# Performance work log

Measured on AMD Instinct MI355X. Metric: run time of the kernel, lower is better.

## Reference

```python
import jax, jax.numpy as jnp
import numpy as np

NUM_QUBITS = 22
NUM_LAYERS = 4
DIM = 2 ** NUM_QUBITS


def _apply_1q(state, U, q):
    # state: flat [2^n]; apply 2x2 unitary U on wire q (wire 0 = most significant)
    s = state.reshape(2 ** q, 2, -1)
    return jnp.einsum('ab,ibj->iaj', U, s).reshape(-1)


def _apply_cnot_adj(state, q):
    # CNOT with control q, target q+1 (adjacent wires)
    s = state.reshape(2 ** q, 2, 2, -1)
    s = jnp.stack([s[:, 0], s[:, 1, ::-1]], axis=1)
    return s.reshape(-1)


def _rot_mats(theta_x, theta_y, theta_z):
    cx = jnp.cos(theta_x / 2).astype(jnp.complex64)
    sx = jnp.sin(theta_x / 2).astype(jnp.complex64)
    RX = jnp.stack([jnp.stack([cx, -1j * sx]), jnp.stack([-1j * sx, cx])])
    cy = jnp.cos(theta_y / 2).astype(jnp.complex64)
    sy = jnp.sin(theta_y / 2).astype(jnp.complex64)
    RY = jnp.stack([jnp.stack([cy, -sy]), jnp.stack([sy, cy])])
    tz = theta_z.astype(jnp.complex64)
    zero = jnp.zeros((), jnp.complex64)
    RZ = jnp.stack([jnp.stack([jnp.exp(-1j * tz / 2), zero]),
                    jnp.stack([zero, jnp.exp(1j * tz / 2)])])
    return RX, RY, RZ


def _circuit(params, state):
    for l in range(NUM_LAYERS):
        for q in range(NUM_QUBITS):
            RX, RY, RZ = _rot_mats(params[l, q, 0], params[l, q, 1], params[l, q, 2])
            state = _apply_1q(state, RX, q)
            state = _apply_1q(state, RY, q)
            state = _apply_1q(state, RZ, q)
        for q in range(NUM_QUBITS - 1):
            state = _apply_cnot_adj(state, q)
    # <Z_q> for each qubit
    probs = jnp.abs(state) ** 2
    expvals = []
    for q in range(NUM_QUBITS):
        p = probs.reshape(2 ** q, 2, -1)
        expvals.append(p[:, 0].sum() - p[:, 1].sum())
    return jnp.stack(expvals).astype(jnp.float32)


def setup_inputs() -> dict:
    key = jax.random.key(0)
    k1, k2, k3 = jax.random.split(key, 3)
    params = jax.random.normal(k1, (NUM_LAYERS, NUM_QUBITS, 3), dtype=jnp.float32)
    state_re = jax.random.normal(k2, (DIM,), dtype=jnp.float32)
    state_im = jax.random.normal(k3, (DIM,), dtype=jnp.float32)
    return {"params": params, "state_re": state_re, "state_im": state_im}


def reference(params, state_re, state_im):
    state = (state_re + 1j * state_im).astype(jnp.complex64)
    state = state / jnp.sqrt(jnp.sum(jnp.abs(state) ** 2))
    return _circuit(params, state)
```

## Files before the change

### kernel.cpp

```cpp
#include <hip/hip_runtime.h>
#include <math.h>

#define NQ 22
#define DIM (1u << NQ)

typedef float v2f __attribute__((ext_vector_type(2)));


__device__ __forceinline__ unsigned igray(unsigned x) {
  x ^= x >> 1; x ^= x >> 2; x ^= x >> 4; x ^= x >> 8; x ^= x >> 16;
  return x;
}

__global__ void k_gates(const float* __restrict__ params, float* __restrict__ U) {
  int t = blockIdx.x * blockDim.x + threadIdx.x;
  if (t >= 88) return;
  const float* p = params + t * 3;
  double hx = 0.5 * (double)p[0], hy = 0.5 * (double)p[1], hz = 0.5 * (double)p[2];
  double cx = cos(hx), sx = sin(hx);
  double cy = cos(hy), sy = sin(hy);
  double cz = cos(hz), sz = sin(hz);
  double m00r = cy * cx, m00i = sy * sx;
  double m01r = -sy * cx, m01i = -cy * sx;
  double m10r = sy * cx, m10i = -cy * sx;
  double m11r = cy * cx, m11i = -sy * sx;
  float* o = U + t * 8;
  o[0] = (float)(cz * m00r + sz * m00i); o[1] = (float)(cz * m00i - sz * m00r);
  o[2] = (float)(cz * m01r + sz * m01i); o[3] = (float)(cz * m01i - sz * m01r);
  o[4] = (float)(cz * m10r - sz * m10i); o[5] = (float)(cz * m10i + sz * m10r);
  o[6] = (float)(cz * m11r - sz * m11i); o[7] = (float)(cz * m11i + sz * m11r);
}

template <int NP>
__device__ __forceinline__ void apply_bit0(v2f RE[NP], v2f IM[NP], const float* __restrict__ u) {
  float u0 = u[0], u1 = u[1], u2 = u[2], u3 = u[3], u4 = u[4], u5 = u[5], u6 = u[6], u7 = u[7];
#pragma unroll
  for (int k = 0; k < NP; ++k) {
    float a0r = RE[k].x, a0i = IM[k].x, a1r = RE[k].y, a1i = IM[k].y;
    float n0r = u0 * a0r - u1 * a0i + u2 * a1r - u3 * a1i;
    float n0i = u0 * a0i + u1 * a0r + u2 * a1i + u3 * a1r;
    float n1r = u4 * a0r - u5 * a0i + u6 * a1r - u7 * a1i;
    float n1i = u4 * a0i + u5 * a0r + u6 * a1i + u7 * a1r;
    RE[k].x = n0r; IM[k].x = n0i; RE[k].y = n1r; IM[k].y = n1i;
  }
}

template <int NP, int PB>
__device__ __forceinline__ void apply_bitP(v2f RE[NP], v2f IM[NP], const float* __restrict__ u) {
  float u0 = u[0], u1 = u[1], u2 = u[2], u3 = u[3], u4 = u[4], u5 = u[5], u6 = u[6], u7 = u[7];
#pragma unroll
  for (int m = 0; m < NP / 2; ++m) {
    int k0 = ((m >> PB) << (PB + 1)) | (m & ((1 << PB) - 1));
    int k1 = k0 | (1 << PB);
    v2f a0r = RE[k0], a0i = IM[k0], a1r = RE[k1], a1i = IM[k1];
    v2f n0r = u0 * a0r - u1 * a0i + u2 * a1r - u3 * a1i;
    v2f n0i = u0 * a0i + u1 * a0r + u2 * a1i + u3 * a1r;
    v2f n1r = u4 * a0r - u5 * a0i + u6 * a1r - u7 * a1i;
    v2f n1i = u4 * a0i + u5 * a0r + u6 * a1i + u7 * a1r;
    RE[k0] = n0r; IM[k0] = n0i; RE[k1] = n1r; IM[k1] = n1i;
  }
}

__device__ __forceinline__ void apply4p(v2f RE[8], v2f IM[8], const float* __restrict__ U,
                                        int l, int wtop) {
  const float* base = U + ((l * 22 + wtop) << 3);
  apply_bit0<8>(RE, IM, base);
  apply_bitP<8, 0>(RE, IM, base - 8);
  apply_bitP<8, 1>(RE, IM, base - 16);
  apply_bitP<8, 2>(RE, IM, base - 24);
}

__device__ __forceinline__ void apply5p(v2f RE[16], v2f IM[16], const float* __restrict__ U,
                                        int l, int wtop) {
  const float* base = U + ((l * 22 + wtop) << 3);
  apply_bit0<16>(RE, IM, base);
  apply_bitP<16, 0>(RE, IM, base - 8);
  apply_bitP<16, 1>(RE, IM, base - 16);
  apply_bitP<16, 2>(RE, IM, base - 24);
  apply_bitP<16, 3>(RE, IM, base - 32);
}

template <typename WI, typename RI>
__device__ __forceinline__ void xchgP(float2* lds2, v2f RE[8], v2f IM[8], WI wi, RI ri) {
  __syncthreads();
#pragma unroll
  for (int d = 0; d < 16; ++d) {
    float2 a;
    if (d & 1) a = make_float2(RE[d >> 1].y, IM[d >> 1].y);
    else       a = make_float2(RE[d >> 1].x, IM[d >> 1].x);
    lds2[wi(d)] = a;
  }
  __syncthreads();
#pragma unroll
  for (int d = 0; d < 16; ++d) {
    float2 a = lds2[ri(d)];
    if (d & 1) { RE[d >> 1].y = a.x; IM[d >> 1].y = a.y; }
    else       { RE[d >> 1].x = a.x; IM[d >> 1].x = a.y; }
  }
}

__global__ __launch_bounds__(256, 4) void k_passA(const float* __restrict__ srcRe,
                                                  const float* __restrict__ srcIm,
                                                  const float2* __restrict__ src2,
                                                  float2* __restrict__ dst,
                                                  const float* __restrict__ U,
                                                  int layer, int first) {
  __shared__ float2 lds2[4096];
  const int t = threadIdx.x;
  const unsigned bid = blockIdx.x;
  const unsigned H = (bid & 7u) * (gridDim.x >> 3) + (bid >> 3);
  v2f RE[8], IM[8];
  if (first) {
    const unsigned jbase = (H << 12) | ((unsigned)t << 4);
    const float4* r4 = (const float4*)(srcRe + jbase);
    const float4* i4 = (const float4*)(srcIm + jbase);
#pragma unroll
    for (int k = 0; k < 4; ++k) {
      float4 r = r4[k], m = i4[k];
      RE[2 * k].x     = r.x; RE[2 * k].y     = r.y;
      IM[2 * k].x     = m.x; IM[2 * k].y     = m.y;
      RE[2 * k + 1].x = r.z; RE[2 * k + 1].y = r.w;
      IM[2 * k + 1].x = m.z; IM[2 * k + 1].y = m.w;
    }
  } else {
    const float4* s4 = (const float4*)(src2 + (((size_t)H << 12) | ((size_t)t << 4)));
#pragma unroll
    for (int k = 0; k < 8; ++k) {
      float4 a = s4[k];
      RE[k].x = a.x; IM[k].x = a.y;
      RE[k].y = a.z; IM[k].y = a.w;
    }
  }
  auto wA = [&](int d) { unsigned j = ((unsigned)t << 4) | (unsigned)d; return (int)(j ^ (j >> 4)); };
  auto rB = [&](int d) { unsigned j = (((unsigned)t >> 4) << 8) | ((unsigned)d << 4) | ((unsigned)t & 15); return (int)(j ^ (j >> 4)); };
  auto rC = [&](int d) { unsigned j = ((unsigned)d << 8) | (unsigned)t; return (int)(j ^ (j >> 4)); };

  apply4p(RE, IM, U, layer, 21);
  xchgP(lds2, RE, IM, wA, rB);
  apply4p(RE, IM, U, layer, 17);
  xchgP(lds2, RE, IM, rB, rC);
  apply4p(RE, IM, U, layer, 13);
  float2* dp = dst + (((size_t)H << 3) | (unsigned)(t & 7));
#pragma unroll
  for (int d = 0; d < 16; ++d) {
    float2 a;
    if (d & 1) a = make_float2(RE[d >> 1].y, IM[d >> 1].y);
    else       a = make_float2(RE[d >> 1].x, IM[d >> 1].x);
    dp[(((size_t)d << 5) | (unsigned)(t >> 3)) << 13] = a;
  }
}

__device__ __forceinline__ int pbf(unsigned e) {
  return (int)(e ^ (((e >> 8) & 7u) << 3));
}

__global__ __launch_bounds__(256, 2) void k_passB(const float2* __restrict__ src,
                                                  float2* __restrict__ dst,
                                                  const float* __restrict__ U,
                                                  int layer) {
  __shared__ float2 lds2[8192];
  const int t = threadIdx.x;
  const unsigned c = (unsigned)(t & 7), u = (unsigned)(t >> 3);
  const unsigned bid = blockIdx.x;
  const unsigned mid = (bid & 7u) * (gridDim.x >> 3) + (bid >> 3);
  const float2* sp = src + (((size_t)mid << 13) | c);
  v2f RE[16], IM[16];
#pragma unroll
  for (int d = 0; d < 32; ++d) {
    unsigned h = u | ((unsigned)d << 5);
    float2 a = sp[(size_t)h << 3];
    if (d & 1) { RE[d >> 1].y = a.x; IM[d >> 1].y = a.y; }
    else       { RE[d >> 1].x = a.x; IM[d >> 1].x = a.y; }
  }
  apply5p(RE, IM, U, layer, 4);
#pragma unroll
  for (int d = 0; d < 32; ++d) {
    unsigned e = ((u | ((unsigned)d << 5)) << 3) | c;
    float2 a;
    if (d & 1) a = make_float2(RE[d >> 1].y, IM[d >> 1].y);
    else       a = make_float2(RE[d >> 1].x, IM[d >> 1].x);
    lds2[pbf(e)] = a;
  }
  __syncthreads();
#pragma unroll
  for (int d = 0; d < 32; ++d) {
    unsigned e = (((unsigned)d | (u << 5)) << 3) | c;
    float2 a = lds2[pbf(e)];
    if (d & 1) { RE[d >> 1].y = a.x; IM[d >> 1].y = a.y; }
    else       { RE[d >> 1].x = a.x; IM[d >> 1].x = a.y; }
  }
  apply5p(RE, IM, U, layer, 9);
  const unsigned Tb = igray((u << 17) | (mid << 3) | c);
#pragma unroll
  for (int d = 0; d < 32; ++d) {
    float2 a;
    if (d & 1) a = make_float2(RE[d >> 1].y, IM[d >> 1].y);
    else       a = make_float2(RE[d >> 1].x, IM[d >> 1].x);
    dst[Tb ^ igray((unsigned)d << 12)] = a;
  }
}

__global__ __launch_bounds__(256, 2) void k_passB_ev(const float2* __restrict__ src,
                                                     const float* __restrict__ U,
                                                     float* __restrict__ partials,
                                                     int layer) {
  __shared__ float2 lds2[8192];
  const int t = threadIdx.x;
  const unsigned c = (unsigned)(t & 7), u = (unsigned)(t >> 3);
  const unsigned bid = blockIdx.x;
  const unsigned mid = (bid & 7u) * (gridDim.x >> 3) + (bid >> 3);
  const float2* sp = src + (((size_t)mid << 13) | c);
  v2f RE[16], IM[16];
#pragma unroll
  for (int d = 0; d < 32; ++d) {
    unsigned h = u | ((unsigned)d << 5);
    float2 a = sp[(size_t)h << 3];
    if (d & 1) { RE[d >> 1].y = a.x; IM[d >> 1].y = a.y; }
    else       { RE[d >> 1].x = a.x; IM[d >> 1].x = a.y; }
  }
  apply5p(RE, IM, U, layer, 4);
#pragma unroll
  for (int d = 0; d < 32; ++d) {
    unsigned e = ((u | ((unsigned)d << 5)) << 3) | c;
    float2 a;
    if (d & 1) a = make_float2(RE[d >> 1].y, IM[d >> 1].y);
    else       a = make_float2(RE[d >> 1].x, IM[d >> 1].x);
    lds2[pbf(e)] = a;
  }
  __syncthreads();
#pragma unroll
  for (int d = 0; d < 32; ++d) {
    unsigned e = (((unsigned)d | (u << 5)) << 3) | c;
    float2 a = lds2[pbf(e)];
    if (d & 1) { RE[d >> 1].y = a.x; IM[d >> 1].y = a.y; }
    else       { RE[d >> 1].x = a.x; IM[d >> 1].x = a.y; }
  }
  apply5p(RE, IM, U, layer, 9);

  v2f PS[16];
#pragma unroll
  for (int k = 0; k < 16; ++k) PS[k] = RE[k] * RE[k] + IM[k] * IM[k];
  v2f S4[8], B4[8];
#pragma unroll
  for (int k = 0; k < 8; ++k) { S4[k] = PS[k] + PS[k + 8]; B4[k] = PS[k] - PS[k + 8]; }
  float Tot = 0.f, W4 = 0.f;
#pragma unroll
  for (int k = 0; k < 8; ++k) { Tot += S4[k].x + S4[k].y; W4 += B4[k].x + B4[k].y; }
  v2f B3[4];
#pragma unroll
  for (int k = 0; k < 4; ++k) B3[k] = B4[k] - B4[k + 4];
  float W3 = (B3[0].x + B3[0].y) + (B3[1].x + B3[1].y) + (B3[2].x + B3[2].y) + (B3[3].x + B3[3].y);
  v2f B2[2];
  B2[0] = B3[0] - B3[2]; B2[1] = B3[1] - B3[3];
  float W2 = (B2[0].x + B2[0].y) + (B2[1].x + B2[1].y);
  v2f B1 = B2[0] - B2[1];
  float W1 = B1.x + B1.y;
  float W0 = B1.x - B1.y;

  unsigned lowfull = (mid << 3) | c;
  unsigned y = lowfull; y ^= y >> 1; y ^= y >> 2; y ^= y >> 4; y ^= y >> 8;
  unsigned pu = (unsigned)__popc(u) & 1u;
  float acc[22];
#pragma unroll
  for (int q = 0; q <= 4; ++q)
    acc[q] = ((unsigned)__popc(u >> (4 - q)) & 1u) ? -Tot : Tot;
  {
    float W[5] = {W0, W1, W2, W3, W4};
#pragma unroll
    for (int q = 5; q <= 9; ++q)
      acc[q] = pu ? -W[9 - q] : W[9 - q];
  }
#pragma unroll
  for (int q = 10; q <= 21; ++q)
    acc[q] = (((y >> (21 - q)) ^ pu) & 1u) ? -W0 : W0;

  __syncthreads();
  float* red = (float*)lds2;
  const int lane = t & 63, wv = t >> 6;
#pragma unroll
  for (int q = 0; q < 22; ++q) {
    float s = acc[q];
    for (int off = 32; off > 0; off >>= 1) s += __shfl_down(s, off, 64);
    if (lane == 0) red[wv * 23 + q] = s;
  }
  {
    float s = Tot;
    for (int off = 32; off > 0; off >>= 1) s += __shfl_down(s, off, 64);
    if (lane == 0) red[wv * 23 + 22] = s;
  }
  __syncthreads();
  if (t < 23) {
    float s = 0.f;
#pragma unroll
    for (int w = 0; w < 4; ++w) s += red[w * 23 + t];
    partials[t * 512 + mid] = s;
  }
}

__global__ void k_final(const float* __restrict__ partials, float* __restrict__ out) {
  __shared__ double res[32];
  const int t = threadIdx.x;
  const int r = t >> 3, l8 = t & 7;
  if (r < 23) {
    double s = 0.0;
    const float* p = partials + r * 512 + l8 * 64;
    for (int k = 0; k < 64; ++k) s += (double)p[k];
    for (int off = 4; off > 0; off >>= 1) s += __shfl_down(s, off, 8);
    if (l8 == 0) res[r] = s;
  }
  __syncthreads();
  if (t < 22) out[t] = (float)(res[t] / res[22]);
}

extern "C" void kernel_launch(void* const* d_in, const int* in_sizes, int n_in,
                              void* d_out, int out_size, void* d_ws, size_t ws_size,
                              hipStream_t stream) {
  const float* params = (const float*)d_in[0];
  const float* sre = (const float*)d_in[1];
  const float* sim = (const float*)d_in[2];
  float* out = (float*)d_out;
  char* ws = (char*)d_ws;
  float* U = (float*)ws;
  float* partials = (float*)(ws + 4096);
  float2* buf0 = (float2*)(ws + 131072);
  float2* buf1 = buf0 + DIM;

  k_gates<<<1, 128, 0, stream>>>(params, U);
  k_passA<<<1024, 256, 0, stream>>>(sre, sim, nullptr, buf0, U, 0, 1);
  k_passB<<<512, 256, 0, stream>>>(buf0, buf1, U, 0);
  for (int l = 1; l < 3; ++l) {
    k_passA<<<1024, 256, 0, stream>>>(nullptr, nullptr, buf1, buf0, U, l, 0);
    k_passB<<<512, 256, 0, stream>>>(buf0, buf1, U, l);
  }
  k_passA<<<1024, 256, 0, stream>>>(nullptr, nullptr, buf1, buf0, U, 3, 0);
  k_passB_ev<<<512, 256, 0, stream>>>(buf0, U, partials, 3);
  k_final<<<1, 256, 0, stream>>>(partials, out);
}
```

Before: 202.3 us.

## Restructure passB to use float4 accesses and three-stage LDS exchange

```diff
diff --git a/kernel.cpp b/kernel.cpp
--- a/kernel.cpp
+++ b/kernel.cpp
@@ -70,16 +70,6 @@
   apply_bitP<8, 2>(RE, IM, base - 24);
 }
 
-__device__ __forceinline__ void apply5p(v2f RE[16], v2f IM[16], const float* __restrict__ U,
-                                        int l, int wtop) {
-  const float* base = U + ((l * 22 + wtop) << 3);
-  apply_bit0<16>(RE, IM, base);
-  apply_bitP<16, 0>(RE, IM, base - 8);
-  apply_bitP<16, 1>(RE, IM, base - 16);
-  apply_bitP<16, 2>(RE, IM, base - 24);
-  apply_bitP<16, 3>(RE, IM, base - 32);
-}
-
 template <typename WI, typename RI>
 __device__ __forceinline__ void xchgP(float2* lds2, v2f RE[8], v2f IM[8], WI wi, RI ri) {
   __syncthreads();
@@ -150,53 +140,84 @@
   }
 }
 
-__device__ __forceinline__ int pbf(unsigned e) {
-  return (int)(e ^ (((e >> 8) & 7u) << 3));
+
+template <bool EV>
+__device__ __forceinline__ void passB_core(const float2* __restrict__ src,
+                                           const float* __restrict__ U,
+                                           float4* lds4, v2f RE[16], v2f IM[16],
+                                           unsigned c2, unsigned u6, unsigned mid,
+                                           int layer) {
+  const float4* sp4 = (const float4*)src + (((size_t)mid << 12) | c2);
+#pragma unroll
+  for (int k = 0; k < 16; ++k) {
+    float4 a = sp4[((unsigned)k << 8) | (u6 << 2)];
+    RE[k].x = a.x; RE[k].y = a.z;
+    IM[k].x = a.y; IM[k].y = a.w;
+  }
+  const float* B = U + layer * 22 * 8;
+  apply_bitP<16, 0>(RE, IM, B + 3 * 8);
+  apply_bitP<16, 1>(RE, IM, B + 2 * 8);
+  apply_bitP<16, 2>(RE, IM, B + 1 * 8);
+  apply_bitP<16, 3>(RE, IM, B + 0 * 8);
+#pragma unroll
+  for (int k = 0; k < 16; ++k) {
+    unsigned s = ((unsigned)k << 8) | (u6 << 2) | c2;
+    s ^= (s >> 6) & 7u;
+    lds4[s] = make_float4(RE[k].x, IM[k].x, RE[k].y, IM[k].y);
+  }
+  __syncthreads();
+#pragma unroll
+  for (int k = 0; k < 16; ++k) {
+    unsigned s = ((unsigned)k << 2) | (u6 << 6) | c2;
+    s ^= (s >> 6) & 7u;
+    float4 a = lds4[s];
+    RE[k].x = a.x; IM[k].x = a.y;
+    RE[k].y = a.z; IM[k].y = a.w;
+  }
+  apply_bitP<16, 0>(RE, IM, B + 9 * 8);
+  apply_bitP<16, 1>(RE, IM, B + 8 * 8);
+  apply_bitP<16, 2>(RE, IM, B + 7 * 8);
+  apply_bitP<16, 3>(RE, IM, B + 6 * 8);
+  __syncthreads();
+#pragma unroll
+  for (int k = 0; k < 16; ++k) {
+    unsigned s = ((unsigned)k << 2) | (u6 << 6) | c2;
+    s ^= (s >> 6) & 7u;
+    lds4[s] = make_float4(RE[k].x, IM[k].x, RE[k].y, IM[k].y);
+  }
+  __syncthreads();
+#pragma unroll
+  for (int k = 0; k < 16; ++k) {
+    unsigned h = (u6 & 15u) | (((unsigned)k & 3u) << 4) | (((unsigned)k >> 2) << 6) | ((u6 >> 4) << 8);
+    unsigned s = (h << 2) | c2;
+    s ^= (s >> 6) & 7u;
+    float4 a = lds4[s];
+    RE[k].x = a.x; IM[k].x = a.y;
+    RE[k].y = a.z; IM[k].y = a.w;
+  }
+  apply_bitP<16, 0>(RE, IM, B + 5 * 8);
+  apply_bitP<16, 1>(RE, IM, B + 4 * 8);
 }
 
 __global__ __launch_bounds__(256, 2) void k_passB(const float2* __restrict__ src,
                                                   float2* __restrict__ dst,
                                                   const float* __restrict__ U,
                                                   int layer) {
-  __shared__ float2 lds2[8192];
+  __shared__ float4 lds4[4096];
   const int t = threadIdx.x;
-  const unsigned c = (unsigned)(t & 7), u = (unsigned)(t >> 3);
+  const unsigned c2 = (unsigned)(t & 3), u6 = (unsigned)(t >> 2);
   const unsigned bid = blockIdx.x;
   const unsigned mid = (bid & 7u) * (gridDim.x >> 3) + (bid >> 3);
-  const float2* sp = src + (((size_t)mid << 13) | c);
   v2f RE[16], IM[16];
-#pragma unroll
-  for (int d = 0; d < 32; ++d) {
-    unsigned h = u | ((unsigned)d << 5);
-    float2 a = sp[(size_t)h << 3];
-    if (d & 1) { RE[d >> 1].y = a.x; IM[d >> 1].y = a.y; }
-    else       { RE[d >> 1].x = a.x; IM[d >> 1].x = a.y; }
-  }
-  apply5p(RE, IM, U, layer, 4);
-#pragma unroll
-  for (int d = 0; d < 32; ++d) {
-    unsigned e = ((u | ((unsigned)d << 5)) << 3) | c;
-    float2 a;
-    if (d & 1) a = make_float2(RE[d >> 1].y, IM[d >> 1].y);
-    else       a = make_float2(RE[d >> 1].x, IM[d >> 1].x);
-    lds2[pbf(e)] = a;
-  }
-  __syncthreads();
-#pragma unroll
-  for (int d = 0; d < 32; ++d) {
-    unsigned e = (((unsigned)d | (u << 5)) << 3) | c;
-    float2 a = lds2[pbf(e)];
-    if (d & 1) { RE[d >> 1].y = a.x; IM[d >> 1].y = a.y; }
-    else       { RE[d >> 1].x = a.x; IM[d >> 1].x = a.y; }
-  }
-  apply5p(RE, IM, U, layer, 9);
-  const unsigned Tb = igray((u << 17) | (mid << 3) | c);
-#pragma unroll
-  for (int d = 0; d < 32; ++d) {
-    float2 a;
-    if (d & 1) a = make_float2(RE[d >> 1].y, IM[d >> 1].y);
-    else       a = make_float2(RE[d >> 1].x, IM[d >> 1].x);
-    dst[Tb ^ igray((unsigned)d << 12)] = a;
+  passB_core<false>(src, U, lds4, RE, IM, c2, u6, mid, layer);
+  const unsigned Tb = igray(((u6 & 15u) << 12) | ((u6 >> 4) << 20) | (mid << 3) | (c2 << 1));
+  float4* dp4 = (float4*)dst;
+#pragma unroll
+  for (int k = 0; k < 16; ++k) {
+    unsigned a2 = Tb ^ igray((((unsigned)k & 3u) << 16) | (((unsigned)k >> 2) << 18));
+    float4 v = (a2 & 1u) ? make_float4(RE[k].y, IM[k].y, RE[k].x, IM[k].x)
+                         : make_float4(RE[k].x, IM[k].x, RE[k].y, IM[k].y);
+    dp4[a2 >> 1] = v;
   }
 }
 
@@ -204,78 +225,61 @@
                                                      const float* __restrict__ U,
                                                      float* __restrict__ partials,
                                                      int layer) {
-  __shared__ float2 lds2[8192];
+  __shared__ float4 lds4[4096];
   const int t = threadIdx.x;
-  const unsigned c = (unsigned)(t & 7), u = (unsigned)(t >> 3);
+  const unsigned c2 = (unsigned)(t & 3), u6 = (unsigned)(t >> 2);
   const unsigned bid = blockIdx.x;
   const unsigned mid = (bid & 7u) * (gridDim.x >> 3) + (bid >> 3);
-  const float2* sp = src + (((size_t)mid << 13) | c);
   v2f RE[16], IM[16];
-#pragma unroll
-  for (int d = 0; d < 32; ++d) {
-    unsigned h = u | ((unsigned)d << 5);
-    float2 a = sp[(size_t)h << 3];
-    if (d & 1) { RE[d >> 1].y = a.x; IM[d >> 1].y = a.y; }
-    else       { RE[d >> 1].x = a.x; IM[d >> 1].x = a.y; }
-  }
-  apply5p(RE, IM, U, layer, 4);
-#pragma unroll
-  for (int d = 0; d < 32; ++d) {
-    unsigned e = ((u | ((unsigned)d << 5)) << 3) | c;
-    float2 a;
-    if (d & 1) a = make_float2(RE[d >> 1].y, IM[d >> 1].y);
-    else       a = make_float2(RE[d >> 1].x, IM[d >> 1].x);
-    lds2[pbf(e)] = a;
-  }
-  __syncthreads();
-#pragma unroll
-  for (int d = 0; d < 32; ++d) {
-    unsigned e = (((unsigned)d | (u << 5)) << 3) | c;
-    float2 a = lds2[pbf(e)];
-    if (d & 1) { RE[d >> 1].y = a.x; IM[d >> 1].y = a.y; }
-    else       { RE[d >> 1].x = a.x; IM[d >> 1].x = a.y; }
-  }
-  apply5p(RE, IM, U, layer, 9);
+  passB_core<true>(src, U, lds4, RE, IM, c2, u6, mid, layer);
 
   v2f PS[16];
 #pragma unroll
   for (int k = 0; k < 16; ++k) PS[k] = RE[k] * RE[k] + IM[k] * IM[k];
-  v2f S4[8], B4[8];
-#pragma unroll
-  for (int k = 0; k < 8; ++k) { S4[k] = PS[k] + PS[k + 8]; B4[k] = PS[k] - PS[k + 8]; }
-  float Tot = 0.f, W4 = 0.f;
-#pragma unroll
-  for (int k = 0; k < 8; ++k) { Tot += S4[k].x + S4[k].y; W4 += B4[k].x + B4[k].y; }
+  float Tot = 0.f, WA = 0.f;
+  v2f B4[8];
+#pragma unroll
+  for (int k = 0; k < 8; ++k) {
+    v2f S = PS[k] + PS[k + 8];
+    Tot += S.x + S.y;
+    B4[k] = PS[k] - PS[k + 8];
+    WA += B4[k].x + B4[k].y;
+  }
   v2f B3[4];
-#pragma unroll
-  for (int k = 0; k < 4; ++k) B3[k] = B4[k] - B4[k + 4];
-  float W3 = (B3[0].x + B3[0].y) + (B3[1].x + B3[1].y) + (B3[2].x + B3[2].y) + (B3[3].x + B3[3].y);
+  float WB = 0.f;
+#pragma unroll
+  for (int k = 0; k < 4; ++k) {
+    B3[k] = B4[k] - B4[k + 4];
+    WB += B3[k].x + B3[k].y;
+  }
   v2f B2[2];
   B2[0] = B3[0] - B3[2]; B2[1] = B3[1] - B3[3];
-  float W2 = (B2[0].x + B2[0].y) + (B2[1].x + B2[1].y);
+  float WC = (B2[0].x + B2[0].y) + (B2[1].x + B2[1].y);
   v2f B1 = B2[0] - B2[1];
-  float W1 = B1.x + B1.y;
-  float W0 = B1.x - B1.y;
-
-  unsigned lowfull = (mid << 3) | c;
-  unsigned y = lowfull; y ^= y >> 1; y ^= y >> 2; y ^= y >> 4; y ^= y >> 8;
-  unsigned pu = (unsigned)__popc(u) & 1u;
+  float W4 = B1.x + B1.y;
+  float W5 = B1.x - B1.y;
+
+  unsigned lowT = (mid << 3) | (c2 << 1);
+  unsigned y = lowT; y ^= y >> 1; y ^= y >> 2; y ^= y >> 4; y ^= y >> 8;
+  unsigned pu = (unsigned)__popc(u6) & 1u;
   float acc[22];
-#pragma unroll
-  for (int q = 0; q <= 4; ++q)
-    acc[q] = ((unsigned)__popc(u >> (4 - q)) & 1u) ? -Tot : Tot;
+  acc[0] = ((u6 >> 5) & 1u) ? -Tot : Tot;
   {
-    float W[5] = {W0, W1, W2, W3, W4};
-#pragma unroll
-    for (int q = 5; q <= 9; ++q)
-      acc[q] = pu ? -W[9 - q] : W[9 - q];
-  }
-#pragma unroll
-  for (int q = 10; q <= 21; ++q)
-    acc[q] = (((y >> (21 - q)) ^ pu) & 1u) ? -W0 : W0;
-
-  __syncthreads();
-  float* red = (float*)lds2;
+    unsigned s01 = (unsigned)__popc(u6 >> 4) & 1u;
+    acc[1] = s01 ? -Tot : Tot;
+    float sg = s01 ? -1.f : 1.f;
+    acc[2] = sg * WA; acc[3] = sg * WB; acc[4] = sg * WC; acc[5] = sg * W4;
+  }
+#pragma unroll
+  for (int q = 6; q <= 9; ++q)
+    acc[q] = ((unsigned)__popc(u6 >> (9 - q)) & 1u) ? -W4 : W4;
+#pragma unroll
+  for (int q = 10; q <= 20; ++q)
+    acc[q] = (((y >> (21 - q)) ^ pu) & 1u) ? -W4 : W4;
+  acc[21] = (((y >> 1) ^ pu) & 1u) ? -W5 : W5;
+
+  __syncthreads();
+  float* red = (float*)lds4;
   const int lane = t & 63, wv = t >> 6;
 #pragma unroll
   for (int q = 0; q < 22; ++q) {
```

Result: slower. 206.9 us (+2.3%).

## Fuse adjacent layer passes to cut full-state global memory sweeps

Applied to the files above, without the earlier changes.

```diff
diff --git a/kernel.cpp b/kernel.cpp
--- a/kernel.cpp
+++ b/kernel.cpp
@@ -99,65 +99,217 @@
   }
 }
 
-__global__ __launch_bounds__(256, 4) void k_passA(const float* __restrict__ srcRe,
-                                                  const float* __restrict__ srcIm,
-                                                  const float2* __restrict__ src2,
-                                                  float2* __restrict__ dst,
-                                                  const float* __restrict__ U,
-                                                  int layer, int first) {
+__device__ __forceinline__ int pbf(unsigned e) {
+  return (int)(e ^ (((e >> 8) & 7u) << 3));
+}
+
+__global__ __launch_bounds__(256, 2) void k_B0(const float* __restrict__ srcRe,
+                                               const float* __restrict__ srcIm,
+                                               float2* __restrict__ dst,
+                                               const float* __restrict__ U) {
+  __shared__ float2 lds2[8192];
+  const int t = threadIdx.x;
+  const unsigned c = (unsigned)(t & 7), u = (unsigned)(t >> 3);
+  const unsigned bid = blockIdx.x;
+  const unsigned mid = (bid & 7u) * (gridDim.x >> 3) + (bid >> 3);
+  const unsigned baselo = (mid << 3) | c;
+  v2f RE[16], IM[16];
+#pragma unroll
+  for (int d = 0; d < 32; ++d) {
+    unsigned h = u | ((unsigned)d << 5);
+    size_t x = ((size_t)h << 12) | baselo;
+    float r = srcRe[x], i = srcIm[x];
+    if (d & 1) { RE[d >> 1].y = r; IM[d >> 1].y = i; }
+    else       { RE[d >> 1].x = r; IM[d >> 1].x = i; }
+  }
+  apply5p(RE, IM, U, 0, 4);
+#pragma unroll
+  for (int d = 0; d < 32; ++d) {
+    unsigned e = ((u | ((unsigned)d << 5)) << 3) | c;
+    float2 a;
+    if (d & 1) a = make_float2(RE[d >> 1].y, IM[d >> 1].y);
+    else       a = make_float2(RE[d >> 1].x, IM[d >> 1].x);
+    lds2[pbf(e)] = a;
+  }
+  __syncthreads();
+#pragma unroll
+  for (int d = 0; d < 32; ++d) {
+    unsigned e = (((unsigned)d | (u << 5)) << 3) | c;
+    float2 a = lds2[pbf(e)];
+    if (d & 1) { RE[d >> 1].y = a.x; IM[d >> 1].y = a.y; }
+    else       { RE[d >> 1].x = a.x; IM[d >> 1].x = a.y; }
+  }
+  apply5p(RE, IM, U, 0, 9);
+#pragma unroll
+  for (int d = 0; d < 32; ++d) {
+    unsigned h = (unsigned)d | (u << 5);
+    size_t x = ((size_t)h << 12) | baselo;
+    float2 a;
+    if (d & 1) a = make_float2(RE[d >> 1].y, IM[d >> 1].y);
+    else       a = make_float2(RE[d >> 1].x, IM[d >> 1].x);
+    dst[x] = a;
+  }
+}
+
+template <int MODE>
+__global__ __launch_bounds__(256, 4) void k_Afused(const float2* __restrict__ src,
+                                                   float2* __restrict__ dst,
+                                                   const float* __restrict__ U,
+                                                   int l) {
   __shared__ float2 lds2[4096];
   const int t = threadIdx.x;
   const unsigned bid = blockIdx.x;
   const unsigned H = (bid & 7u) * (gridDim.x >> 3) + (bid >> 3);
+  const unsigned Pm = ((unsigned)(__popc(H) & 1)) << 11;
   v2f RE[8], IM[8];
-  if (first) {
-    const unsigned jbase = (H << 12) | ((unsigned)t << 4);
-    const float4* r4 = (const float4*)(srcRe + jbase);
-    const float4* i4 = (const float4*)(srcIm + jbase);
-#pragma unroll
-    for (int k = 0; k < 4; ++k) {
-      float4 r = r4[k], m = i4[k];
-      RE[2 * k].x     = r.x; RE[2 * k].y     = r.y;
-      IM[2 * k].x     = m.x; IM[2 * k].y     = m.y;
-      RE[2 * k + 1].x = r.z; RE[2 * k + 1].y = r.w;
-      IM[2 * k + 1].x = m.z; IM[2 * k + 1].y = m.w;
-    }
-  } else {
-    const float4* s4 = (const float4*)(src2 + (((size_t)H << 12) | ((size_t)t << 4)));
-#pragma unroll
-    for (int k = 0; k < 8; ++k) {
-      float4 a = s4[k];
-      RE[k].x = a.x; IM[k].x = a.y;
-      RE[k].y = a.z; IM[k].y = a.w;
-    }
+  const float4* s4 = (const float4*)(src + (((size_t)H << 12) | ((size_t)t << 4)));
+#pragma unroll
+  for (int k = 0; k < 8; ++k) {
+    float4 a = s4[k];
+    RE[k].x = a.x; IM[k].x = a.y;
+    RE[k].y = a.z; IM[k].y = a.w;
   }
   auto wA = [&](int d) { unsigned j = ((unsigned)t << 4) | (unsigned)d; return (int)(j ^ (j >> 4)); };
   auto rB = [&](int d) { unsigned j = (((unsigned)t >> 4) << 8) | ((unsigned)d << 4) | ((unsigned)t & 15); return (int)(j ^ (j >> 4)); };
   auto rC = [&](int d) { unsigned j = ((unsigned)d << 8) | (unsigned)t; return (int)(j ^ (j >> 4)); };
-
-  apply4p(RE, IM, U, layer, 21);
+  auto rT = [&](int d) { unsigned m = ((unsigned)t << 4) | (unsigned)d;
+                         unsigned j = (m ^ (m >> 1)) ^ Pm; return (int)(j ^ (j >> 4)); };
+
+  apply4p(RE, IM, U, l, 21);
   xchgP(lds2, RE, IM, wA, rB);
-  apply4p(RE, IM, U, layer, 17);
+  apply4p(RE, IM, U, l, 17);
   xchgP(lds2, RE, IM, rB, rC);
-  apply4p(RE, IM, U, layer, 13);
-  float2* dp = dst + (((size_t)H << 3) | (unsigned)(t & 7));
-#pragma unroll
-  for (int d = 0; d < 16; ++d) {
-    float2 a;
-    if (d & 1) a = make_float2(RE[d >> 1].y, IM[d >> 1].y);
-    else       a = make_float2(RE[d >> 1].x, IM[d >> 1].x);
-    dp[(((size_t)d << 5) | (unsigned)(t >> 3)) << 13] = a;
-  }
-}
-
-__device__ __forceinline__ int pbf(unsigned e) {
-  return (int)(e ^ (((e >> 8) & 7u) << 3));
-}
-
-__global__ __launch_bounds__(256, 2) void k_passB(const float2* __restrict__ src,
-                                                  float2* __restrict__ dst,
-                                                  const float* __restrict__ U,
-                                                  int layer) {
+  apply4p(RE, IM, U, l, 13);
+  xchgP(lds2, RE, IM, rC, rT);
+  apply4p(RE, IM, U, l + 1, 21);
+  xchgP(lds2, RE, IM, wA, rB);
+  apply4p(RE, IM, U, l + 1, 17);
+  xchgP(lds2, RE, IM, rB, rC);
+  apply4p(RE, IM, U, l + 1, 13);
+  const unsigned GH = igray(H);
+  if (MODE == 0) {
+    float2* dp = dst + ((GH << 3) | ((unsigned)t & 3));
+#pragma unroll
+    for (int d = 0; d < 16; ++d) {
+      float2 a;
+      if (d & 1) a = make_float2(RE[d >> 1].y, IM[d >> 1].y);
+      else       a = make_float2(RE[d >> 1].x, IM[d >> 1].x);
+      unsigned addr = (((((unsigned)d & 7u) << 6) | ((unsigned)t >> 2)) << 13)
+                    | ((((unsigned)d >> 3) & 1u) << 2);
+      dp[addr] = a;
+    }
+  } else {
+    float2* dp = dst + ((GH << 3) | ((unsigned)t & 7));
+#pragma unroll
+    for (int d = 0; d < 16; ++d) {
+      float2 a;
+      if (d & 1) a = make_float2(RE[d >> 1].y, IM[d >> 1].y);
+      else       a = make_float2(RE[d >> 1].x, IM[d >> 1].x);
+      unsigned addr = ((((unsigned)d << 5) | ((unsigned)t >> 3)) << 13);
+      dp[addr] = a;
+    }
+  }
+}
+
+__device__ __forceinline__ int phi3(unsigned o) {
+  return (int)(o ^ (((o >> 8) & 7u) << 3));
+}
+
+__global__ __launch_bounds__(256, 2) void k_Bfused(const float2* __restrict__ src,
+                                                   float2* __restrict__ dst,
+                                                   const float* __restrict__ U) {
+  __shared__ float2 lds2[8192];
+  const int t = threadIdx.x;
+  const unsigned low2 = (unsigned)(t & 3);
+  const unsigned u6 = (unsigned)t >> 2;
+  const unsigned uA = (u6 >> 1) & 31u, uB = u6 & 1u;
+  const unsigned bid = blockIdx.x;
+  const unsigned mid = (bid & 7u) * (gridDim.x >> 3) + (bid >> 3);
+  v2f RE[16], IM[16];
+  const float2* sp = src + (((size_t)mid << 13) | (uA << 3) | (uB << 2) | low2);
+#pragma unroll
+  for (int s = 0; s < 32; ++s) {
+    float2 a = sp[(size_t)s << 8];
+    if (s & 1) { RE[s >> 1].y = a.x; IM[s >> 1].y = a.y; }
+    else       { RE[s >> 1].x = a.x; IM[s >> 1].x = a.y; }
+  }
+  apply5p(RE, IM, U, 1, 4);
+#pragma unroll
+  for (int s = 0; s < 32; ++s) {
+    unsigned o = (((((unsigned)s << 5) | uA) << 3)) | (uB << 2) | low2;
+    float2 a;
+    if (s & 1) a = make_float2(RE[s >> 1].y, IM[s >> 1].y);
+    else       a = make_float2(RE[s >> 1].x, IM[s >> 1].x);
+    lds2[phi3(o)] = a;
+  }
+  __syncthreads();
+#pragma unroll
+  for (int s = 0; s < 32; ++s) {
+    unsigned o = ((((uA << 5) | (unsigned)s) << 3)) | (uB << 2) | low2;
+    float2 a = lds2[phi3(o)];
+    if (s & 1) { RE[s >> 1].y = a.x; IM[s >> 1].y = a.y; }
+    else       { RE[s >> 1].x = a.x; IM[s >> 1].x = a.y; }
+  }
+  __syncthreads();
+  apply5p(RE, IM, U, 1, 9);
+#pragma unroll
+  for (int s = 0; s < 32; ++s) {
+    unsigned o = ((((uA << 5) | (unsigned)s) << 3)) | (uB << 2) | low2;
+    float2 a;
+    if (s & 1) a = make_float2(RE[s >> 1].y, IM[s >> 1].y);
+    else       a = make_float2(RE[s >> 1].x, IM[s >> 1].x);
+    lds2[phi3(o)] = a;
+  }
+  __syncthreads();
+#pragma unroll
+  for (int s = 0; s < 32; ++s) {
+    unsigned M = uB | ((unsigned)s << 1) | (uA << 6);
+    unsigned Y = M ^ (M >> 1);
+    unsigned o = ((Y >> 1) << 3) | ((Y & 1u) << 2) | low2;
+    float2 a = lds2[phi3(o)];
+    if (s & 1) { RE[s >> 1].y = a.x; IM[s >> 1].y = a.y; }
+    else       { RE[s >> 1].x = a.x; IM[s >> 1].x = a.y; }
+  }
+  __syncthreads();
+  apply5p(RE, IM, U, 2, 9);
+#pragma unroll
+  for (int s = 0; s < 32; ++s) {
+    unsigned M = uB | ((unsigned)s << 1) | (uA << 6);
+    unsigned Y = M ^ (M >> 1);
+    unsigned o = ((Y >> 1) << 3) | ((Y & 1u) << 2) | low2;
+    float2 a;
+    if (s & 1) a = make_float2(RE[s >> 1].y, IM[s >> 1].y);
+    else       a = make_float2(RE[s >> 1].x, IM[s >> 1].x);
+    lds2[phi3(o)] = a;
+  }
+  __syncthreads();
+#pragma unroll
+  for (int s = 0; s < 32; ++s) {
+    unsigned M = uB | (uA << 1) | ((unsigned)s << 6);
+    unsigned Y = M ^ (M >> 1);
+    unsigned o = ((Y >> 1) << 3) | ((Y & 1u) << 2) | low2;
+    float2 a = lds2[phi3(o)];
+    if (s & 1) { RE[s >> 1].y = a.x; IM[s >> 1].y = a.y; }
+    else       { RE[s >> 1].x = a.x; IM[s >> 1].x = a.y; }
+  }
+  apply5p(RE, IM, U, 2, 4);
+  const unsigned S9 = igray(mid);
+  const unsigned CONSTK = (S9 << 2) | ((S9 & 1u) * 3u);
+  const unsigned lowmix = (low2 & 1u) ^ (3u * ((low2 >> 1) & 1u));
+  const unsigned zlow = CONSTK ^ (uB ? 0xFFFu : 0u) ^ lowmix;
+#pragma unroll
+  for (int s = 0; s < 32; ++s) {
+    unsigned z = ((uA | ((unsigned)s << 5)) << 12) | zlow;
+    float2 a;
+    if (s & 1) a = make_float2(RE[s >> 1].y, IM[s >> 1].y);
+    else       a = make_float2(RE[s >> 1].x, IM[s >> 1].x);
+    dst[z] = a;
+  }
+}
+
+__global__ __launch_bounds__(256, 2) void k_Bev(const float2* __restrict__ src,
+                                                const float* __restrict__ U,
+                                                float* __restrict__ partials) {
   __shared__ float2 lds2[8192];
   const int t = threadIdx.x;
   const unsigned c = (unsigned)(t & 7), u = (unsigned)(t >> 3);
@@ -172,7 +324,7 @@
     if (d & 1) { RE[d >> 1].y = a.x; IM[d >> 1].y = a.y; }
     else       { RE[d >> 1].x = a.x; IM[d >> 1].x = a.y; }
   }
-  apply5p(RE, IM, U, layer, 4);
+  apply5p(RE, IM, U, 3, 4);
 #pragma unroll
   for (int d = 0; d < 32; ++d) {
     unsigned e = ((u | ((unsigned)d << 5)) << 3) | c;
@@ -189,53 +341,7 @@
     if (d & 1) { RE[d >> 1].y = a.x; IM[d >> 1].y = a.y; }
     else       { RE[d >> 1].x = a.x; IM[d >> 1].x = a.y; }
   }
-  apply5p(RE, IM, U, layer, 9);
-  const unsigned Tb = igray((u << 17) | (mid << 3) | c);
-#pragma unroll
-  for (int d = 0; d < 32; ++d) {
-    float2 a;
-    if (d & 1) a = make_float2(RE[d >> 1].y, IM[d >> 1].y);
-    else       a = make_float2(RE[d >> 1].x, IM[d >> 1].x);
-    dst[Tb ^ igray((unsigned)d << 12)] = a;
-  }
-}
-
-__global__ __launch_bounds__(256, 2) void k_passB_ev(const float2* __restrict__ src,
-                                                     const float* __restrict__ U,
-                                                     float* __restrict__ partials,
-                                                     int layer) {
-  __shared__ float2 lds2[8192];
-  const int t = threadIdx.x;
-  const unsigned c = (unsigned)(t & 7), u = (unsigned)(t >> 3);
-  const unsigned bid = blockIdx.x;
-  const unsigned mid = (bid & 7u) * (gridDim.x >> 3) + (bid >> 3);
-  const float2* sp = src + (((size_t)mid << 13) | c);
-  v2f RE[16], IM[16];
-#pragma unroll
-  for (int d = 0; d < 32; ++d) {
-    unsigned h = u | ((unsigned)d << 5);
-    float2 a = sp[(size_t)h << 3];
-    if (d & 1) { RE[d >> 1].y = a.x; IM[d >> 1].y = a.y; }
-    else       { RE[d >> 1].x = a.x; IM[d >> 1].x = a.y; }
-  }
-  apply5p(RE, IM, U, layer, 4);
-#pragma unroll
-  for (int d = 0; d < 32; ++d) {
-    unsigned e = ((u | ((unsigned)d << 5)) << 3) | c;
-    float2 a;
-    if (d & 1) a = make_float2(RE[d >> 1].y, IM[d >> 1].y);
-    else       a = make_float2(RE[d >> 1].x, IM[d >> 1].x);
-    lds2[pbf(e)] = a;
-  }
-  __syncthreads();
-#pragma unroll
-  for (int d = 0; d < 32; ++d) {
-    unsigned e = (((unsigned)d | (u << 5)) << 3) | c;
-    float2 a = lds2[pbf(e)];
-    if (d & 1) { RE[d >> 1].y = a.x; IM[d >> 1].y = a.y; }
-    else       { RE[d >> 1].x = a.x; IM[d >> 1].x = a.y; }
-  }
-  apply5p(RE, IM, U, layer, 9);
+  apply5p(RE, IM, U, 3, 9);
 
   v2f PS[16];
 #pragma unroll
@@ -326,13 +432,10 @@
   float2* buf1 = buf0 + DIM;
 
   k_gates<<<1, 128, 0, stream>>>(params, U);
-  k_passA<<<1024, 256, 0, stream>>>(sre, sim, nullptr, buf0, U, 0, 1);
-  k_passB<<<512, 256, 0, stream>>>(buf0, buf1, U, 0);
-  for (int l = 1; l < 3; ++l) {
-    k_passA<<<1024, 256, 0, stream>>>(nullptr, nullptr, buf1, buf0, U, l, 0);
-    k_passB<<<512, 256, 0, stream>>>(buf0, buf1, U, l);
-  }
-  k_passA<<<1024, 256, 0, stream>>>(nullptr, nullptr, buf1, buf0, U, 3, 0);
-  k_passB_ev<<<512, 256, 0, stream>>>(buf0, U, partials, 3);
+  k_B0<<<512, 256, 0, stream>>>(sre, sim, buf0, U);
+  k_Afused<0><<<1024, 256, 0, stream>>>(buf0, buf1, U, 0);
+  k_Bfused<<<512, 256, 0, stream>>>(buf1, buf0, U);
+  k_Afused<1><<<1024, 256, 0, stream>>>(buf0, buf1, U, 2);
+  k_Bev<<<512, 256, 0, stream>>>(buf1, U, partials);
   k_final<<<1, 256, 0, stream>>>(partials, out);
 }
```

Result: faster. 189.1 us (-6.5%).
